# Performance work log

Hardware: AMD Instinct MI355X
Metric: run time of the kernel (lower is better)

Reference implementation:

```python
import jax, jax.numpy as jnp
import numpy as np

D_MODEL, N_STATE, L_MAX, BATCH = 256, 64, 2048, 16

def _to_c(x):
    return jax.lax.complex(x[..., 0], x[..., 1])

def setup_inputs() -> dict:
    key = jax.random.key(0)
    k_u, k_ct_r, k_ct_i, k_step = jax.random.split(key, 4)
    n, d = N_STATE, D_MODEL
    # --- HiPPO DPLR init (numpy, matches torch hippo_dplr) ---
    P = np.sqrt(1.0 + 2.0 * np.arange(1, n + 1, dtype=np.float64))
    A = np.tril(np.outer(P, P)) - np.diag(np.arange(1, n + 1, dtype=np.float64))
    A = -A
    p = 0.5 * np.sqrt(2.0 * np.arange(1, n + 1, dtype=np.float64) + 1.0)
    Ap = (A + np.outer(p, p)).astype(np.complex64)
    lam, V = np.linalg.eig(Ap)
    p_rot = V.conj().T @ p.astype(np.complex64)
    p_ri = np.stack([p_rot.real, p_rot.imag], -1).astype(np.float32)          # (n,2)
    lambda_ri = np.stack([lam.real, lam.imag], -1).astype(np.float32)         # (n,2)
    # --- B init: sqrt(2k+1), repeated over channels, zero imag ---
    B_r = np.sqrt(2.0 * np.arange(1, n + 1) + 1.0).astype(np.float32)
    B_ri = np.stack([np.tile(B_r, (d, 1)), np.zeros((d, n), np.float32)], -1) # (d,n,2)
    # --- Ct: xavier-normal complex ---
    std = float(np.sqrt(2.0 / (d + n)))
    Ct_r = jax.random.normal(k_ct_r, (d, n), jnp.float32) * (std / np.sqrt(2.0))
    Ct_i = jax.random.normal(k_ct_i, (d, n), jnp.float32) * (std / np.sqrt(2.0))
    Ct_ri = jnp.stack([Ct_r, Ct_i], -1)                                        # (d,n,2)
    Dp = jnp.ones((1, 1, d), jnp.float32)
    log_step = jax.random.uniform(k_step, (d,), jnp.float32) * (
        np.log(0.1) - np.log(0.001)) + np.log(0.001)
    u = jax.random.normal(k_u, (BATCH, L_MAX, d), jnp.float32)
    return {"u": u, "p_ri": jnp.asarray(p_ri), "lambda_ri": jnp.asarray(lambda_ri),
            "B_ri": jnp.asarray(B_ri), "Ct_ri": Ct_ri, "Dp": Dp, "log_step": log_step}

def reference(u, p_ri, lambda_ri, B_ri, Ct_ri, Dp, log_step):
    p = _to_c(p_ri)          # (n,)
    lam = _to_c(lambda_ri)   # (n,)
    B = _to_c(B_ri)          # (d,n)
    Ct = _to_c(Ct_ri)        # (d,n)
    L = u.shape[1]
    omega = jnp.exp(2j * jnp.pi * jnp.arange(L) / L).astype(jnp.complex64)  # (L,)
    step = jnp.exp(log_step)                                               # (d,)
    g = (2.0 / step)[:, None] * ((1.0 - omega) / (1.0 + omega))[None, :]   # (d,L)
    c = 2.0 / (1.0 + omega)                                                # (L,)
    inv = 1.0 / (g[:, :, None] - lam[None, None, :])                       # (d,L,n)
    k00 = jnp.einsum('dn,dln->dl', Ct.conj() * B, inv)
    k01 = jnp.einsum('dn,dln->dl', Ct.conj() * p[None, :], inv)
    k10 = jnp.einsum('dn,dln->dl', p.conj()[None, :] * B, inv)
    k11 = jnp.einsum('n,dln->dl', p.conj() * p, inv)
    at_roots = c[None, :] * (k00 - k01 * k10 / (1.0 + k11))                # (d,L)
    out = jnp.fft.ifft(at_roots, n=L, axis=-1)
    order = jnp.concatenate([jnp.zeros((1,), jnp.int32), jnp.arange(L - 1, 0, -1)])
    K = out[:, order].real[None]                                           # (1,d,L)
    # causal FFT convolution
    ud = jnp.fft.rfft(jnp.pad(u, ((0, 0), (0, L), (0, 0))), axis=1)        # (B,L+1,d)
    Kd = jnp.fft.rfft(jnp.pad(K, ((0, 0), (0, 0), (0, L))), axis=-1)       # (1,d,L+1)
    y = jnp.fft.irfft(jnp.transpose(ud, (0, 2, 1)) * Kd, axis=-1)[..., :L]
    y = jnp.transpose(y, (0, 2, 1)).astype(u.dtype)                        # (B,L,d)
    return y + Dp * u
```

## Files before the change

### kernel.cpp

```cpp
#include <hip/hip_runtime.h>
#include <math.h>

#define LLEN   2048
#define NFFT   4096
#define DMODEL 256
#define NSTATE 64
#define NBATCH 16
#define PI_F   3.14159265358979323846f

#define PADIDX(a) ((a) + ((a) >> 4))
#define LDSN (NFFT + (NFFT >> 4))

__device__ inline float frcp(float x) { return __builtin_amdgcn_rcpf(x); }

#define RADIX4(ar0,ai0,ar1,ai1,ar2,ai2,ar3,ai3,S) do {                      \
    float s0r=(ar0)+(ar2), s0i=(ai0)+(ai2);                                 \
    float s1r=(ar0)-(ar2), s1i=(ai0)-(ai2);                                 \
    float s2r=(ar1)+(ar3), s2i=(ai1)+(ai3);                                 \
    float s3r=(ar1)-(ar3), s3i=(ai1)-(ai3);                                 \
    (ar0)=s0r+s2r; (ai0)=s0i+s2i;                                           \
    (ar2)=s0r-s2r; (ai2)=s0i-s2i;                                           \
    (ar1)=s1r-(S)*s3i; (ai1)=s1i+(S)*s3r;                                   \
    (ar3)=s1r+(S)*s3i; (ai3)=s1i-(S)*s3r;                                   \
} while (0)

template<int SIGN>
__device__ inline void dft16(float xr[16], float xi[16]) {
    const float S = (float)SIGN;
    const float C1 = 0.9238795325112867f, S1 = 0.3826834323650898f;
    const float C2 = 0.7071067811865476f;
    RADIX4(xr[0],xi[0], xr[4],xi[4], xr[8],xi[8],  xr[12],xi[12], S);
    RADIX4(xr[1],xi[1], xr[5],xi[5], xr[9],xi[9],  xr[13],xi[13], S);
    RADIX4(xr[2],xi[2], xr[6],xi[6], xr[10],xi[10],xr[14],xi[14], S);
    RADIX4(xr[3],xi[3], xr[7],xi[7], xr[11],xi[11],xr[15],xi[15], S);
#define TW(idx, wr_, wi_) { float tr = xr[idx]*(wr_) - xi[idx]*(wi_);       \
    xi[idx] = xr[idx]*(wi_) + xi[idx]*(wr_); xr[idx] = tr; }
    TW(5,  C1,  S*S1);
    TW(6,  C2,  S*C2);
    TW(7,  S1,  S*C1);
    TW(9,  C2,  S*C2);
    TW(10, 0.f, S);
    TW(11, -C2, S*C2);
    TW(13, S1,  S*C1);
    TW(14, -C2, S*C2);
    TW(15, -C1, -S*S1);
#undef TW
    RADIX4(xr[0],xi[0],  xr[1],xi[1],  xr[2],xi[2],  xr[3],xi[3],  S);
    RADIX4(xr[4],xi[4],  xr[5],xi[5],  xr[6],xi[6],  xr[7],xi[7],  S);
    RADIX4(xr[8],xi[8],  xr[9],xi[9],  xr[10],xi[10],xr[11],xi[11],S);
    RADIX4(xr[12],xi[12],xr[13],xi[13],xr[14],xi[14],xr[15],xi[15],S);
}

template<int SIGN>
__device__ inline void dft8(float xr[8], float xi[8]) {
    const float S = (float)SIGN;
    const float C2 = 0.7071067811865476f;
    RADIX4(xr[0],xi[0], xr[2],xi[2], xr[4],xi[4], xr[6],xi[6], S);
    RADIX4(xr[1],xi[1], xr[3],xi[3], xr[5],xi[5], xr[7],xi[7], S);
    { float tr = xr[3]*C2 - xi[3]*(S*C2); xi[3] = xr[3]*(S*C2) + xi[3]*C2; xr[3] = tr; }
    { float tr = -S*xi[5]; xi[5] = S*xr[5]; xr[5] = tr; }
    { float tr = xr[7]*(-C2) - xi[7]*(S*C2); xi[7] = xr[7]*(S*C2) + xi[7]*(-C2); xr[7] = tr; }
    float br[8], bi[8];
#pragma unroll
    for (int k = 0; k < 4; ++k) {
        br[k]   = xr[2*k] + xr[2*k+1]; bi[k]   = xi[2*k] + xi[2*k+1];
        br[k+4] = xr[2*k] - xr[2*k+1]; bi[k+4] = xi[2*k] - xi[2*k+1];
    }
#pragma unroll
    for (int k = 0; k < 8; ++k) { xr[k] = br[k]; xi[k] = bi[k]; }
}

__device__ inline void store16(float* Xr, float* Xi, const float xr[16],
                               const float xi[16], int base, int L) {
#pragma unroll
    for (int k0 = 0; k0 < 4; ++k0)
#pragma unroll
        for (int k2 = 0; k2 < 4; ++k2) {
            int a = base + (k0 + 4 * k2) * L;
            int s = 4 * k0 + k2;
            Xr[PADIDX(a)] = xr[s];
            Xi[PADIDX(a)] = xi[s];
        }
}

template<int SIGN>
__device__ inline void fft_stage16(float* Xr, float* Xi, int j, int m, int L, bool active) {
    float xr[16], xi[16];
    const int p = j & (L - 1);
    if (active) {
#pragma unroll
        for (int t = 0; t < 16; ++t) {
            int a = j + t * m;
            xr[t] = Xr[PADIDX(a)]; xi[t] = Xi[PADIDX(a)];
        }
        float sn, cn;
        __sincosf(((float)SIGN * 2.f * PI_F) * (float)p / (float)(16 * L), &sn, &cn);
        float wr = cn, wi = sn;
#pragma unroll
        for (int t = 1; t < 16; ++t) {
            float tr = xr[t]*wr - xi[t]*wi;
            xi[t] = xr[t]*wi + xi[t]*wr; xr[t] = tr;
            float nr = wr*cn - wi*sn; wi = wr*sn + wi*cn; wr = nr;
        }
        dft16<SIGN>(xr, xi);
    }
    __syncthreads();
    if (active) store16(Xr, Xi, xr, xi, 16 * j - 15 * p, L);
    __syncthreads();
}

template<int SIGN, bool ZHI>
__device__ inline void fft4096(float* Xr, float* Xi, int tid) {
    {
        float xr[16], xi[16];
#pragma unroll
        for (int t = 0; t < 16; ++t) {
            if (ZHI && t >= 8) { xr[t] = 0.f; xi[t] = 0.f; }
            else { int a = tid + t * 256; xr[t] = Xr[PADIDX(a)]; xi[t] = Xi[PADIDX(a)]; }
        }
        dft16<SIGN>(xr, xi);
        __syncthreads();
        store16(Xr, Xi, xr, xi, 16 * tid, 1);
        __syncthreads();
    }
    fft_stage16<SIGN>(Xr, Xi, tid, 256, 16, true);
    fft_stage16<SIGN>(Xr, Xi, tid, 256, 256, true);
}

template<int SIGN>
__device__ inline void fft2048(float* Xr, float* Xi, int tid) {
    {
        float xr[8], xi[8];
#pragma unroll
        for (int t = 0; t < 8; ++t) {
            int a = tid + t * 256;
            xr[t] = Xr[PADIDX(a)]; xi[t] = Xi[PADIDX(a)];
        }
        dft8<SIGN>(xr, xi);
        __syncthreads();
#pragma unroll
        for (int u = 0; u < 8; ++u) {
            int a = 8 * tid + u;
            Xr[PADIDX(a)] = xr[u]; Xi[PADIDX(a)] = xi[u];
        }
        __syncthreads();
    }
    fft_stage16<SIGN>(Xr, Xi, tid, 128, 8,   tid < 128);
    fft_stage16<SIGN>(Xr, Xi, tid, 128, 128, tid < 128);
}

__global__ __launch_bounds__(256) void k_transpose_u(const float* __restrict__ u,
                                                     float* __restrict__ ut) {
    __shared__ float tile[32][33];
    const int bt0 = blockIdx.x * 32, ch0 = blockIdx.y * 32;
    const int tx = threadIdx.x, ty = threadIdx.y;
    for (int k = 0; k < 4; ++k) {
        const int r = ty + 8 * k;
        tile[r][tx] = u[(size_t)(bt0 + r) * DMODEL + ch0 + tx];
    }
    __syncthreads();
    for (int k = 0; k < 4; ++k) {
        const int r = ty + 8 * k;
        ut[(size_t)(ch0 + r) * (NBATCH * LLEN) + bt0 + tx] = tile[tx][r];
    }
}

__global__ __launch_bounds__(256) void k_atroots(const float* __restrict__ p_ri,
                                                 const float* __restrict__ lambda_ri,
                                                 const float* __restrict__ B_ri,
                                                 const float* __restrict__ Ct_ri,
                                                 const float* __restrict__ log_step,
                                                 float2* __restrict__ ar_out) {
    __shared__ float4 c0[NSTATE];
    __shared__ float4 c1[NSTATE];
    __shared__ float2 lam[NSTATE];
    const int d = blockIdx.x >> 3;
    const int l = ((blockIdx.x & 7) << 8) | threadIdx.x;
    const int tid = threadIdx.x;
    if (tid < NSTATE) {
        const int n = tid;
        const float px = p_ri[2*n], py = p_ri[2*n+1];
        lam[n] = make_float2(lambda_ri[2*n], lambda_ri[2*n+1]);
        const float Bx = B_ri[(d*NSTATE+n)*2], By = B_ri[(d*NSTATE+n)*2+1];
        const float Cx = Ct_ri[(d*NSTATE+n)*2], Cy = Ct_ri[(d*NSTATE+n)*2+1];
        c0[n] = make_float4(Cx*Bx + Cy*By, Cx*By - Cy*Bx,
                            Cx*px + Cy*py, Cx*py - Cy*px);
        c1[n] = make_float4(px*Bx + py*By, px*By - py*Bx, px*px + py*py, 0.f);
    }
    __syncthreads();

    const float tos = 2.f * __expf(-log_step[d]);
    float sn, cs;
    sincosf(2.f * PI_F * (float)l / (float)LLEN, &sn, &cs);
    const float opx = 1.f + cs, opy = sn;
    const float omx = 1.f - cs, omy = -sn;
    const float inv_op = frcp(opx*opx + opy*opy);
    const float gx = tos * (omx*opx + omy*opy) * inv_op;
    const float gy = tos * (omy*opx - omx*opy) * inv_op;
    const float ccx = 2.f * opx * inv_op, ccy = -2.f * opy * inv_op;

    float k00x = 0, k00y = 0, k01x = 0, k01y = 0;
    float k10x = 0, k10y = 0, k11x = 0, k11y = 0;
    for (int n = 0; n < NSTATE; ++n) {
        const float2 lm = lam[n];
        const float dx = gx - lm.x, dy = gy - lm.y;
        const float idn = frcp(dx*dx + dy*dy);
        const float ix = dx * idn, iy = -dy * idn;
        const float4 a = c0[n];
        const float4 b = c1[n];
        k00x += a.x*ix - a.y*iy;  k00y += a.x*iy + a.y*ix;
        k01x += a.z*ix - a.w*iy;  k01y += a.z*iy + a.w*ix;
        k10x += b.x*ix - b.y*iy;  k10y += b.x*iy + b.y*ix;
        k11x += b.z*ix;           k11y += b.z*iy;
    }
    const float nx = k01x*k10x - k01y*k10y;
    const float ny = k01x*k10y + k01y*k10x;
    const float dpx = 1.f + k11x, dpy = k11y;
    const float idq = frcp(dpx*dpx + dpy*dpy);
    const float qx = (nx*dpx + ny*dpy) * idq;
    const float qy = (ny*dpx - nx*dpy) * idq;
    const float rx = k00x - qx, ry = k00y - qy;
    ar_out[(size_t)d * LLEN + l] = make_float2(ccx*rx - ccy*ry, ccx*ry + ccy*rx);
}

__global__ __launch_bounds__(256, 4) void k_khat(const float2* __restrict__ ar_in,
                                                 float2* __restrict__ Khat) {
    __shared__ float Xr[LDSN], Xi[LDSN];
    const int d = blockIdx.x, tid = threadIdx.x;
    for (int l = tid; l < LLEN; l += 256) {
        float2 v = ar_in[(size_t)d * LLEN + l];
        Xr[PADIDX(l)] = v.x; Xi[PADIDX(l)] = v.y;
    }
    __syncthreads();
    fft2048<-1>(Xr, Xi, tid);
    for (int l = tid; l < LLEN; l += 256) {
        const int pl = PADIDX(l);
        Xr[pl] = Xr[pl] * (1.f / (float)LLEN);
        Xi[pl] = 0.f;
    }
    __syncthreads();
    fft4096<-1, true>(Xr, Xi, tid);
    for (int f = tid; f < NFFT; f += 256)
        Khat[(size_t)d * NFFT + f] = make_float2(Xr[PADIDX(f)], Xi[PADIDX(f)]);
}

__global__ __launch_bounds__(256, 4) void k_conv(const float* __restrict__ ut,
                                                 const float2* __restrict__ Khat,
                                                 float* __restrict__ yt) {
    __shared__ float Xr[LDSN], Xi[LDSN];
    const int ch = blockIdx.x >> 3, pair = blockIdx.x & 7, tid = threadIdx.x;
    const float* u0 = ut + (size_t)ch * (NBATCH * LLEN) + (size_t)(2 * pair) * LLEN;
    const float* u1 = u0 + LLEN;
    for (int i = tid; i < LLEN; i += 256) {
        Xr[PADIDX(i)] = u0[i]; Xi[PADIDX(i)] = u1[i];
    }
    __syncthreads();
    fft4096<-1, true>(Xr, Xi, tid);

    const float2* H = Khat + (size_t)ch * NFFT;
    for (int f = tid; f <= NFFT / 2; f += 256) {
        const int fb = (NFFT - f) & (NFFT - 1);
        const int pf = PADIDX(f), pfb = PADIDX(fb);
        const float zax = Xr[pf], zay = Xi[pf];
        const float zbx = Xr[pfb], zby = Xi[pfb];
        const float u0x = 0.5f * (zax + zbx), u0y = 0.5f * (zay - zby);
        const float u1x = 0.5f * (zay + zby), u1y = -0.5f * (zax - zbx);
        const float2 Ha = H[f];
        const float y0x = u0x*Ha.x - u0y*Ha.y, y0y = u0x*Ha.y + u0y*Ha.x;
        const float y1x = u1x*Ha.x - u1y*Ha.y, y1y = u1x*Ha.y + u1y*Ha.x;
        Xr[pf] = y0x - y1y; Xi[pf] = y0y + y1x;
        if (fb != f) {
            const float2 Hb = H[fb];
            const float z0x = u0x*Hb.x + u0y*Hb.y, z0y = u0x*Hb.y - u0y*Hb.x;
            const float z1x = u1x*Hb.x + u1y*Hb.y, z1y = u1x*Hb.y - u1y*Hb.x;
            Xr[pfb] = z0x - z1y; Xi[pfb] = z0y + z1x;
        }
    }
    __syncthreads();
    fft4096<+1, false>(Xr, Xi, tid);

    float* y0o = yt + (size_t)ch * (NBATCH * LLEN) + (size_t)(2 * pair) * LLEN;
    float* y1o = y0o + LLEN;
    const float sc = 1.f / (float)NFFT;
    for (int i = tid; i < LLEN; i += 256) {
        y0o[i] = Xr[PADIDX(i)] * sc;
        y1o[i] = Xi[PADIDX(i)] * sc;
    }
}

__global__ __launch_bounds__(256) void k_transpose_y(const float* __restrict__ yt,
                                                     const float* __restrict__ u,
                                                     const float* __restrict__ Dp,
                                                     float* __restrict__ out) {
    __shared__ float tile[32][33];
    const int bt0 = blockIdx.x * 32, ch0 = blockIdx.y * 32;
    const int tx = threadIdx.x, ty = threadIdx.y;
    for (int k = 0; k < 4; ++k) {
        const int r = ty + 8 * k;
        tile[r][tx] = yt[(size_t)(ch0 + r) * (NBATCH * LLEN) + bt0 + tx];
    }
    __syncthreads();
    const float dp = Dp[ch0 + tx];
    for (int k = 0; k < 4; ++k) {
        const int r = ty + 8 * k;
        const size_t idx = (size_t)(bt0 + r) * DMODEL + ch0 + tx;
        out[idx] = tile[tx][r] + dp * u[idx];
    }
}

extern "C" void kernel_launch(void* const* d_in, const int* in_sizes, int n_in,
                              void* d_out, int out_size, void* d_ws, size_t ws_size,
                              hipStream_t stream) {
    const float* u         = (const float*)d_in[0];
    const float* p_ri      = (const float*)d_in[1];
    const float* lambda_ri = (const float*)d_in[2];
    const float* B_ri      = (const float*)d_in[3];
    const float* Ct_ri     = (const float*)d_in[4];
    const float* Dp        = (const float*)d_in[5];
    const float* log_step  = (const float*)d_in[6];
    float* out = (float*)d_out;

    float2* Khat = (float2*)d_ws;
    float*  yt   = (float*)((char*)d_ws + (size_t)DMODEL * NFFT * sizeof(float2));
    float2* ar   = (float2*)yt;
    float*  ut   = out;

    k_transpose_u<<<dim3(NBATCH * LLEN / 32, DMODEL / 32), dim3(32, 8), 0, stream>>>(u, ut);
    k_atroots<<<DMODEL * 8, 256, 0, stream>>>(p_ri, lambda_ri, B_ri, Ct_ri, log_step, ar);
    k_khat<<<DMODEL, 256, 0, stream>>>(ar, Khat);
    k_conv<<<DMODEL * (NBATCH / 2), 256, 0, stream>>>(ut, Khat, yt);
    k_transpose_y<<<dim3(NBATCH * LLEN / 32, DMODEL / 32), dim3(32, 8), 0, stream>>>(yt, u, Dp, out);
}
```

Measured before the change: 190.9 us.

## Fuse transpose, at-roots and kernel FFT into one pre-kernel; switch LDS to float2

Merges the u transpose, the at-roots evaluation and the K-hat FFT into a single launch, so the at-roots intermediate never goes through global memory and two launches disappear. The FFT LDS buffers become interleaved float2, twiddles are computed by squaring instead of serial rotation, and the final inverse FFT stage skips stores for the discarded upper half. The 1/N scaling moves into Khat, and k_conv loads its input with float4. Risks include higher register pressure from 4-wide at-roots batching and a larger LDS footprint in the transpose blocks of the merged kernel.

```diff
diff --git a/kernel.cpp b/kernel.cpp
--- a/kernel.cpp
+++ b/kernel.cpp
@@ -70,113 +70,127 @@
     for (int k = 0; k < 8; ++k) { xr[k] = br[k]; xi[k] = bi[k]; }
 }
 
-__device__ inline void store16(float* Xr, float* Xi, const float xr[16],
-                               const float xi[16], int base, int L) {
-#pragma unroll
-    for (int k0 = 0; k0 < 4; ++k0)
-#pragma unroll
-        for (int k2 = 0; k2 < 4; ++k2) {
-            int a = base + (k0 + 4 * k2) * L;
-            int s = 4 * k0 + k2;
-            Xr[PADIDX(a)] = xr[s];
-            Xi[PADIDX(a)] = xi[s];
-        }
-}
-
 template<int SIGN>
-__device__ inline void fft_stage16(float* Xr, float* Xi, int j, int m, int L, bool active) {
+__device__ inline void tw_apply16(float xr[16], float xi[16], float ang) {
+    float wr[16], wi[16];
+    __sincosf(ang, &wi[1], &wr[1]);
+#pragma unroll
+    for (int k = 1; k < 8; ++k) {
+        wr[2*k]   = wr[k]*wr[k] - wi[k]*wi[k];
+        wi[2*k]   = 2.f * wr[k] * wi[k];
+        wr[2*k+1] = wr[k]*wr[k+1] - wi[k]*wi[k+1];
+        wi[2*k+1] = wr[k]*wi[k+1] + wi[k]*wr[k+1];
+    }
+#pragma unroll
+    for (int t = 1; t < 16; ++t) {
+        float tr = xr[t]*wr[t] - xi[t]*wi[t];
+        xi[t] = xr[t]*wi[t] + xi[t]*wr[t];
+        xr[t] = tr;
+    }
+}
+
+template<int SIGN, int M, int L, bool PRUNE>
+__device__ inline void stage16(float2* X, int j, bool active) {
     float xr[16], xi[16];
     const int p = j & (L - 1);
     if (active) {
 #pragma unroll
         for (int t = 0; t < 16; ++t) {
-            int a = j + t * m;
-            xr[t] = Xr[PADIDX(a)]; xi[t] = Xi[PADIDX(a)];
-        }
-        float sn, cn;
-        __sincosf(((float)SIGN * 2.f * PI_F) * (float)p / (float)(16 * L), &sn, &cn);
-        float wr = cn, wi = sn;
-#pragma unroll
-        for (int t = 1; t < 16; ++t) {
-            float tr = xr[t]*wr - xi[t]*wi;
-            xi[t] = xr[t]*wi + xi[t]*wr; xr[t] = tr;
-            float nr = wr*cn - wi*sn; wi = wr*sn + wi*cn; wr = nr;
-        }
+            float2 v = X[PADIDX(j + t * M)];
+            xr[t] = v.x; xi[t] = v.y;
+        }
+        tw_apply16<SIGN>(xr, xi, ((float)SIGN * 2.f * PI_F / (float)(16 * L)) * (float)p);
         dft16<SIGN>(xr, xi);
     }
     __syncthreads();
-    if (active) store16(Xr, Xi, xr, xi, 16 * j - 15 * p, L);
-    __syncthreads();
-}
-
-template<int SIGN, bool ZHI>
-__device__ inline void fft4096(float* Xr, float* Xi, int tid) {
-    {
-        float xr[16], xi[16];
-#pragma unroll
-        for (int t = 0; t < 16; ++t) {
-            if (ZHI && t >= 8) { xr[t] = 0.f; xi[t] = 0.f; }
-            else { int a = tid + t * 256; xr[t] = Xr[PADIDX(a)]; xi[t] = Xi[PADIDX(a)]; }
-        }
-        dft16<SIGN>(xr, xi);
+    if (active) {
+        const int base = 16 * j - 15 * p;
+#pragma unroll
+        for (int k0 = 0; k0 < 4; ++k0)
+#pragma unroll
+            for (int k2 = 0; k2 < 4; ++k2) {
+                const int u = k0 + 4 * k2;
+                if (!PRUNE || u < 8) {
+                    const int a = base + u * L;
+                    X[PADIDX(a)] = make_float2(xr[4*k0+k2], xi[4*k0+k2]);
+                }
+            }
+    }
+    __syncthreads();
+}
+
+template<int SIGN, bool ZHI, bool PRUNE>
+__device__ inline void fft4096_f2(float2* X, int tid) {
+    float xr[16], xi[16];
+#pragma unroll
+    for (int t = 0; t < 16; ++t) {
+        if (ZHI && t >= 8) { xr[t] = 0.f; xi[t] = 0.f; }
+        else { float2 v = X[PADIDX(tid + t * 256)]; xr[t] = v.x; xi[t] = v.y; }
+    }
+    dft16<SIGN>(xr, xi);
+    __syncthreads();
+#pragma unroll
+    for (int k0 = 0; k0 < 4; ++k0)
+#pragma unroll
+        for (int k2 = 0; k2 < 4; ++k2)
+            X[PADIDX(16 * tid + k0 + 4 * k2)] = make_float2(xr[4*k0+k2], xi[4*k0+k2]);
+    __syncthreads();
+    stage16<SIGN, 256, 16,  false>(X, tid, true);
+    stage16<SIGN, 256, 256, PRUNE>(X, tid, true);
+}
+
+template<int SIGN>
+__device__ inline void fft2048_f2(float2* X, int tid) {
+    float xr[8], xi[8];
+#pragma unroll
+    for (int t = 0; t < 8; ++t) {
+        float2 v = X[PADIDX(tid + t * 256)];
+        xr[t] = v.x; xi[t] = v.y;
+    }
+    dft8<SIGN>(xr, xi);
+    __syncthreads();
+#pragma unroll
+    for (int u = 0; u < 8; ++u)
+        X[PADIDX(8 * tid + u)] = make_float2(xr[u], xi[u]);
+    __syncthreads();
+    stage16<SIGN, 128, 8,   false>(X, tid, tid < 128);
+    stage16<SIGN, 128, 128, false>(X, tid, tid < 128);
+}
+
+__global__ __launch_bounds__(256, 4) void k_pre(const float* __restrict__ u,
+                                                const float* __restrict__ p_ri,
+                                                const float* __restrict__ lambda_ri,
+                                                const float* __restrict__ B_ri,
+                                                const float* __restrict__ Ct_ri,
+                                                const float* __restrict__ log_step,
+                                                float* __restrict__ ut,
+                                                float2* __restrict__ Khat) {
+    __shared__ float2 X[LDSN];
+    __shared__ float4 c0[NSTATE], c1[NSTATE];
+    __shared__ float2 lam[NSTATE];
+    const int tid = threadIdx.x;
+
+    if (blockIdx.x >= DMODEL) {
+        const int blk = blockIdx.x - DMODEL;
+        const int bt0 = (blk & 1023) * 32;
+        const int ch0 = (blk >> 10) * 32;
+        float* tile = (float*)X;
+        const int tx = tid & 31, ty = tid >> 5;
+#pragma unroll
+        for (int k = 0; k < 4; ++k) {
+            const int r = ty + 8 * k;
+            tile[r * 33 + tx] = u[(size_t)(bt0 + r) * DMODEL + ch0 + tx];
+        }
         __syncthreads();
-        store16(Xr, Xi, xr, xi, 16 * tid, 1);
-        __syncthreads();
-    }
-    fft_stage16<SIGN>(Xr, Xi, tid, 256, 16, true);
-    fft_stage16<SIGN>(Xr, Xi, tid, 256, 256, true);
-}
-
-template<int SIGN>
-__device__ inline void fft2048(float* Xr, float* Xi, int tid) {
-    {
-        float xr[8], xi[8];
-#pragma unroll
-        for (int t = 0; t < 8; ++t) {
-            int a = tid + t * 256;
-            xr[t] = Xr[PADIDX(a)]; xi[t] = Xi[PADIDX(a)];
-        }
-        dft8<SIGN>(xr, xi);
-        __syncthreads();
-#pragma unroll
-        for (int u = 0; u < 8; ++u) {
-            int a = 8 * tid + u;
-            Xr[PADIDX(a)] = xr[u]; Xi[PADIDX(a)] = xi[u];
-        }
-        __syncthreads();
-    }
-    fft_stage16<SIGN>(Xr, Xi, tid, 128, 8,   tid < 128);
-    fft_stage16<SIGN>(Xr, Xi, tid, 128, 128, tid < 128);
-}
-
-__global__ __launch_bounds__(256) void k_transpose_u(const float* __restrict__ u,
-                                                     float* __restrict__ ut) {
-    __shared__ float tile[32][33];
-    const int bt0 = blockIdx.x * 32, ch0 = blockIdx.y * 32;
-    const int tx = threadIdx.x, ty = threadIdx.y;
-    for (int k = 0; k < 4; ++k) {
-        const int r = ty + 8 * k;
-        tile[r][tx] = u[(size_t)(bt0 + r) * DMODEL + ch0 + tx];
-    }
-    __syncthreads();
-    for (int k = 0; k < 4; ++k) {
-        const int r = ty + 8 * k;
-        ut[(size_t)(ch0 + r) * (NBATCH * LLEN) + bt0 + tx] = tile[tx][r];
-    }
-}
-
-__global__ __launch_bounds__(256) void k_atroots(const float* __restrict__ p_ri,
-                                                 const float* __restrict__ lambda_ri,
-                                                 const float* __restrict__ B_ri,
-                                                 const float* __restrict__ Ct_ri,
-                                                 const float* __restrict__ log_step,
-                                                 float2* __restrict__ ar_out) {
-    __shared__ float4 c0[NSTATE];
-    __shared__ float4 c1[NSTATE];
-    __shared__ float2 lam[NSTATE];
-    const int d = blockIdx.x >> 3;
-    const int l = ((blockIdx.x & 7) << 8) | threadIdx.x;
-    const int tid = threadIdx.x;
+#pragma unroll
+        for (int k = 0; k < 4; ++k) {
+            const int r = ty + 8 * k;
+            ut[(size_t)(ch0 + r) * (NBATCH * LLEN) + bt0 + tx] = tile[tx * 33 + r];
+        }
+        return;
+    }
+
+    const int d = blockIdx.x;
     if (tid < NSTATE) {
         const int n = tid;
         const float px = p_ri[2*n], py = p_ri[2*n+1];
@@ -190,108 +204,122 @@
     __syncthreads();
 
     const float tos = 2.f * __expf(-log_step[d]);
-    float sn, cs;
-    sincosf(2.f * PI_F * (float)l / (float)LLEN, &sn, &cs);
-    const float opx = 1.f + cs, opy = sn;
-    const float omx = 1.f - cs, omy = -sn;
-    const float inv_op = frcp(opx*opx + opy*opy);
-    const float gx = tos * (omx*opx + omy*opy) * inv_op;
-    const float gy = tos * (omy*opx - omx*opy) * inv_op;
-    const float ccx = 2.f * opx * inv_op, ccy = -2.f * opy * inv_op;
-
-    float k00x = 0, k00y = 0, k01x = 0, k01y = 0;
-    float k10x = 0, k10y = 0, k11x = 0, k11y = 0;
-    for (int n = 0; n < NSTATE; ++n) {
-        const float2 lm = lam[n];
-        const float dx = gx - lm.x, dy = gy - lm.y;
-        const float idn = frcp(dx*dx + dy*dy);
-        const float ix = dx * idn, iy = -dy * idn;
-        const float4 a = c0[n];
-        const float4 b = c1[n];
-        k00x += a.x*ix - a.y*iy;  k00y += a.x*iy + a.y*ix;
-        k01x += a.z*ix - a.w*iy;  k01y += a.z*iy + a.w*ix;
-        k10x += b.x*ix - b.y*iy;  k10y += b.x*iy + b.y*ix;
-        k11x += b.z*ix;           k11y += b.z*iy;
-    }
-    const float nx = k01x*k10x - k01y*k10y;
-    const float ny = k01x*k10y + k01y*k10x;
-    const float dpx = 1.f + k11x, dpy = k11y;
-    const float idq = frcp(dpx*dpx + dpy*dpy);
-    const float qx = (nx*dpx + ny*dpy) * idq;
-    const float qy = (ny*dpx - nx*dpy) * idq;
-    const float rx = k00x - qx, ry = k00y - qy;
-    ar_out[(size_t)d * LLEN + l] = make_float2(ccx*rx - ccy*ry, ccx*ry + ccy*rx);
-}
-
-__global__ __launch_bounds__(256, 4) void k_khat(const float2* __restrict__ ar_in,
-                                                 float2* __restrict__ Khat) {
-    __shared__ float Xr[LDSN], Xi[LDSN];
-    const int d = blockIdx.x, tid = threadIdx.x;
+    for (int kk = 0; kk < 8; kk += 4) {
+        float gx[4], gy[4], ccx[4], ccy[4];
+#pragma unroll
+        for (int jj = 0; jj < 4; ++jj) {
+            const int l = tid + (kk + jj) * 256;
+            float sn, cs;
+            sincosf(2.f * PI_F * (float)l / (float)LLEN, &sn, &cs);
+            const float opx = 1.f + cs, opy = sn;
+            const float omx = 1.f - cs, omy = -sn;
+            const float inv_op = frcp(opx*opx + opy*opy);
+            gx[jj] = tos * (omx*opx + omy*opy) * inv_op;
+            gy[jj] = tos * (omy*opx - omx*opy) * inv_op;
+            ccx[jj] = 2.f * opx * inv_op; ccy[jj] = -2.f * opy * inv_op;
+        }
+        float k00x[4] = {0,0,0,0}, k00y[4] = {0,0,0,0};
+        float k01x[4] = {0,0,0,0}, k01y[4] = {0,0,0,0};
+        float k10x[4] = {0,0,0,0}, k10y[4] = {0,0,0,0};
+        float k11x[4] = {0,0,0,0}, k11y[4] = {0,0,0,0};
+        for (int n = 0; n < NSTATE; ++n) {
+            const float4 a = c0[n];
+            const float4 b = c1[n];
+            const float2 lm = lam[n];
+#pragma unroll
+            for (int jj = 0; jj < 4; ++jj) {
+                const float dx = gx[jj] - lm.x, dy = gy[jj] - lm.y;
+                const float idn = frcp(dx*dx + dy*dy);
+                const float ix = dx * idn, iy = -dy * idn;
+                k00x[jj] += a.x*ix - a.y*iy;  k00y[jj] += a.x*iy + a.y*ix;
+                k01x[jj] += a.z*ix - a.w*iy;  k01y[jj] += a.z*iy + a.w*ix;
+                k10x[jj] += b.x*ix - b.y*iy;  k10y[jj] += b.x*iy + b.y*ix;
+                k11x[jj] += b.z*ix;           k11y[jj] += b.z*iy;
+            }
+        }
+#pragma unroll
+        for (int jj = 0; jj < 4; ++jj) {
+            const float nx = k01x[jj]*k10x[jj] - k01y[jj]*k10y[jj];
+            const float ny = k01x[jj]*k10y[jj] + k01y[jj]*k10x[jj];
+            const float dpx = 1.f + k11x[jj], dpy = k11y[jj];
+            const float idq = frcp(dpx*dpx + dpy*dpy);
+            const float qx = (nx*dpx + ny*dpy) * idq;
+            const float qy = (ny*dpx - nx*dpy) * idq;
+            const float rx = k00x[jj] - qx, ry = k00y[jj] - qy;
+            X[PADIDX(tid + (kk + jj) * 256)] =
+                make_float2(ccx[jj]*rx - ccy[jj]*ry, ccx[jj]*ry + ccy[jj]*rx);
+        }
+    }
+    __syncthreads();
+
+    fft2048_f2<-1>(X, tid);
     for (int l = tid; l < LLEN; l += 256) {
-        float2 v = ar_in[(size_t)d * LLEN + l];
-        Xr[PADIDX(l)] = v.x; Xi[PADIDX(l)] = v.y;
-    }
-    __syncthreads();
-    fft2048<-1>(Xr, Xi, tid);
-    for (int l = tid; l < LLEN; l += 256) {
-        const int pl = PADIDX(l);
-        Xr[pl] = Xr[pl] * (1.f / (float)LLEN);
-        Xi[pl] = 0.f;
-    }
-    __syncthreads();
-    fft4096<-1, true>(Xr, Xi, tid);
-    for (int f = tid; f < NFFT; f += 256)
-        Khat[(size_t)d * NFFT + f] = make_float2(Xr[PADIDX(f)], Xi[PADIDX(f)]);
+        const int q = PADIDX(l);
+        float2 v = X[q];
+        X[q] = make_float2(v.x * (1.f / (float)LLEN), 0.f);
+    }
+    __syncthreads();
+    fft4096_f2<-1, true, false>(X, tid);
+    const float isc = 1.f / (float)NFFT;
+    for (int f = tid; f < NFFT; f += 256) {
+        float2 v = X[PADIDX(f)];
+        Khat[(size_t)d * NFFT + f] = make_float2(v.x * isc, v.y * isc);
+    }
 }
 
 __global__ __launch_bounds__(256, 4) void k_conv(const float* __restrict__ ut,
                                                  const float2* __restrict__ Khat,
                                                  float* __restrict__ yt) {
-    __shared__ float Xr[LDSN], Xi[LDSN];
+    __shared__ float2 X[LDSN];
     const int ch = blockIdx.x >> 3, pair = blockIdx.x & 7, tid = threadIdx.x;
-    const float* u0 = ut + (size_t)ch * (NBATCH * LLEN) + (size_t)(2 * pair) * LLEN;
-    const float* u1 = u0 + LLEN;
-    for (int i = tid; i < LLEN; i += 256) {
-        Xr[PADIDX(i)] = u0[i]; Xi[PADIDX(i)] = u1[i];
-    }
-    __syncthreads();
-    fft4096<-1, true>(Xr, Xi, tid);
+    const float4* u0 = (const float4*)(ut + (size_t)ch * (NBATCH * LLEN) + (size_t)(2 * pair) * LLEN);
+    const float4* u1 = u0 + LLEN / 4;
+#pragma unroll
+    for (int k = 0; k < 2; ++k) {
+        const int v4 = tid + k * 256;
+        const float4 a = u0[v4], b = u1[v4];
+        const int base = 4 * v4;
+        X[PADIDX(base + 0)] = make_float2(a.x, b.x);
+        X[PADIDX(base + 1)] = make_float2(a.y, b.y);
+        X[PADIDX(base + 2)] = make_float2(a.z, b.z);
+        X[PADIDX(base + 3)] = make_float2(a.w, b.w);
+    }
+    __syncthreads();
+    fft4096_f2<-1, true, false>(X, tid);
 
     const float2* H = Khat + (size_t)ch * NFFT;
     for (int f = tid; f <= NFFT / 2; f += 256) {
         const int fb = (NFFT - f) & (NFFT - 1);
-        const int pf = PADIDX(f), pfb = PADIDX(fb);
-        const float zax = Xr[pf], zay = Xi[pf];
-        const float zbx = Xr[pfb], zby = Xi[pfb];
-        const float u0x = 0.5f * (zax + zbx), u0y = 0.5f * (zay - zby);
-        const float u1x = 0.5f * (zay + zby), u1y = -0.5f * (zax - zbx);
+        const float2 Za = X[PADIDX(f)], Zb = X[PADIDX(fb)];
+        const float u0x = 0.5f * (Za.x + Zb.x), u0y = 0.5f * (Za.y - Zb.y);
+        const float u1x = 0.5f * (Za.y + Zb.y), u1y = -0.5f * (Za.x - Zb.x);
         const float2 Ha = H[f];
         const float y0x = u0x*Ha.x - u0y*Ha.y, y0y = u0x*Ha.y + u0y*Ha.x;
         const float y1x = u1x*Ha.x - u1y*Ha.y, y1y = u1x*Ha.y + u1y*Ha.x;
-        Xr[pf] = y0x - y1y; Xi[pf] = y0y + y1x;
+        X[PADIDX(f)] = make_float2(y0x - y1y, y0y + y1x);
         if (fb != f) {
             const float2 Hb = H[fb];
             const float z0x = u0x*Hb.x + u0y*Hb.y, z0y = u0x*Hb.y - u0y*Hb.x;
             const float z1x = u1x*Hb.x + u1y*Hb.y, z1y = u1x*Hb.y - u1y*Hb.x;
-            Xr[pfb] = z0x - z1y; Xi[pfb] = z0y + z1x;
-        }
-    }
-    __syncthreads();
-    fft4096<+1, false>(Xr, Xi, tid);
+            X[PADIDX(fb)] = make_float2(z0x - z1y, z0y + z1x);
+        }
+    }
+    __syncthreads();
+    fft4096_f2<+1, false, true>(X, tid);
 
     float* y0o = yt + (size_t)ch * (NBATCH * LLEN) + (size_t)(2 * pair) * LLEN;
     float* y1o = y0o + LLEN;
-    const float sc = 1.f / (float)NFFT;
     for (int i = tid; i < LLEN; i += 256) {
-        y0o[i] = Xr[PADIDX(i)] * sc;
-        y1o[i] = Xi[PADIDX(i)] * sc;
-    }
-}
-
-__global__ __launch_bounds__(256) void k_transpose_y(const float* __restrict__ yt,
-                                                     const float* __restrict__ u,
-                                                     const float* __restrict__ Dp,
-                                                     float* __restrict__ out) {
+        const float2 v = X[PADIDX(i)];
+        y0o[i] = v.x;
+        y1o[i] = v.y;
+    }
+}
+
+__global__ __launch_bounds__(256) void k_post(const float* __restrict__ yt,
+                                              const float* __restrict__ u,
+                                              const float* __restrict__ Dp,
+                                              float* __restrict__ out) {
     __shared__ float tile[32][33];
     const int bt0 = blockIdx.x * 32, ch0 = blockIdx.y * 32;
     const int tx = threadIdx.x, ty = threadIdx.y;
@@ -322,12 +350,9 @@
 
     float2* Khat = (float2*)d_ws;
     float*  yt   = (float*)((char*)d_ws + (size_t)DMODEL * NFFT * sizeof(float2));
-    float2* ar   = (float2*)yt;
     float*  ut   = out;
 
-    k_transpose_u<<<dim3(NBATCH * LLEN / 32, DMODEL / 32), dim3(32, 8), 0, stream>>>(u, ut);
-    k_atroots<<<DMODEL * 8, 256, 0, stream>>>(p_ri, lambda_ri, B_ri, Ct_ri, log_step, ar);
-    k_khat<<<DMODEL, 256, 0, stream>>>(ar, Khat);
+    k_pre<<<DMODEL + 8192, 256, 0, stream>>>(u, p_ri, lambda_ri, B_ri, Ct_ri, log_step, ut, Khat);
     k_conv<<<DMODEL * (NBATCH / 2), 256, 0, stream>>>(ut, Khat, yt);
-    k_transpose_y<<<dim3(NBATCH * LLEN / 32, DMODEL / 32), dim3(32, 8), 0, stream>>>(yt, u, Dp, out);
-}
+    k_post<<<dim3(NBATCH * LLEN / 32, DMODEL / 32), dim3(32, 8), 0, stream>>>(yt, u, Dp, out);
+}
```

Measured after the change: 185.3 us. 1.03x faster.
